# Kernel optimization log

Measured on AMD Instinct MI355X. Metric: run time of the kernel, lower is better.

Reference implementation:

```python
import jax, jax.numpy as jnp
import numpy as np

EPS = 1e-8


def setup_inputs() -> dict:
    key = jax.random.key(0)
    k1, k2, k3, k4 = jax.random.split(key, 4)
    b, c_in, c_out, h, w_, k = 16, 512, 512, 64, 64, 3
    return {
        "x": jax.random.normal(k1, (b, c_in, h, w_), dtype=jnp.float32),
        "w": jax.random.normal(k2, (b, 512), dtype=jnp.float32),
        "weight": jax.random.normal(k3, (c_out, c_in, k, k), dtype=jnp.float32),
        "affine_w": jax.random.normal(k4, (c_in, 512), dtype=jnp.float32) * 0.02,
        "affine_b": jnp.zeros((c_in,), dtype=jnp.float32),
    }


def reference(x, w, weight, affine_w, affine_b):
    # x: [b, c_in, h, w]; w: [b, 512]; weight: [c_out, c_in, k, k]
    b = x.shape[0]
    # per-sample modulation scale: [b, c_in]
    s = w @ affine_w.T + affine_b + 1.0
    # modulated weights: [b, c_out, c_in, k, k]
    wgt = weight[None] * s[:, None, :, None, None]
    # demodulation: rsqrt of sum over (c_in, kh, kw)
    d = jax.lax.rsqrt(jnp.sum(wgt ** 2, axis=(2, 3, 4)) + EPS)  # [b, c_out]
    wgt = wgt * d[:, :, None, None, None]

    def conv_one(x_i, w_i):
        # x_i: [c_in, h, w] -> [1, c_in, h, w]; w_i: [c_out, c_in, k, k]
        out = jax.lax.conv_general_dilated(
            x_i[None], w_i, window_strides=(1, 1), padding="SAME",
            dimension_numbers=("NCHW", "OIHW", "NCHW"))
        return out[0]

    return jax.vmap(conv_one)(x, wgt)  # [b, c_out, h, w]
```

## Files before the change

### kernel.cpp

```cpp
#include <hip/hip_runtime.h>
#include <cstdint>

typedef __bf16 bf16_t;
typedef __attribute__((ext_vector_type(8))) __bf16 bf16x8;
typedef __attribute__((ext_vector_type(4))) float f32x4;

#define MC_EPS 1e-8f

__device__ __forceinline__ void async_ld16(const bf16_t* g, bf16_t* l) {
  __builtin_amdgcn_global_load_lds(
      (const __attribute__((address_space(1))) void*)g,
      (__attribute__((address_space(3))) void*)l, 16, 0, 0);
}

__global__ void s_kernel(const float* __restrict__ w, const float* __restrict__ aw,
                         const float* __restrict__ ab, float* __restrict__ s) {
  int ci = blockIdx.x, tid = threadIdx.x;
  int b = tid >> 4, part = tid & 15;
  const float* ar = aw + (ci << 9);
  const float* wr = w + (b << 9);
  float acc = 0.f;
  for (int j = part; j < 512; j += 16) acc += wr[j] * ar[j];
  for (int off = 8; off; off >>= 1) acc += __shfl_down(acc, off, 64);
  if (part == 0) s[(b << 9) + ci] = acc + ab[ci] + 1.0f;
}

__global__ void prep_w_kernel(const float* __restrict__ wgt, float* __restrict__ wsq,
                              bf16_t* __restrict__ w_t) {
  int idx = blockIdx.x * 256 + threadIdx.x;
  const float* p = wgt + (size_t)idx * 9;
  float v[9];
  float a = 0.f;
#pragma unroll
  for (int j = 0; j < 9; ++j) { v[j] = p[j]; a += v[j] * v[j]; }
  wsq[idx] = a;
#pragma unroll
  for (int j = 0; j < 9; ++j) w_t[((size_t)j << 18) + idx] = (bf16_t)v[j];
}

__global__ void d_kernel(const float* __restrict__ wsq, const float* __restrict__ s,
                         float* __restrict__ d) {
  int co = blockIdx.x, tid = threadIdx.x;
  int b = tid >> 4, part = tid & 15;
  const float* wr = wsq + (co << 9);
  const float* sr = s + (b << 9);
  float acc = 0.f;
  for (int j = part; j < 512; j += 16) { float sv = sr[j]; acc += wr[j] * sv * sv; }
  for (int off = 8; off; off >>= 1) acc += __shfl_down(acc, off, 64);
  if (part == 0) d[(b << 9) + co] = rsqrtf(acc + MC_EPS);
}

__global__ void halo_kernel(bf16_t* __restrict__ xp) {
  int gid = blockIdx.x * 256 + threadIdx.x;
  if (gid >= 16 * 260 * 64) return;
  int cg = gid & 63;
  int p = (gid >> 6) % 260;
  int b = (gid >> 6) / 260;
  int h, w;
  if (p < 66)       { h = 0;       w = p; }
  else if (p < 132) { h = 65;      w = p - 66; }
  else if (p < 196) { h = p - 131; w = 0; }
  else              { h = p - 195; w = 65; }
  uint4 z = {0u, 0u, 0u, 0u};
  *(uint4*)&xp[((size_t)(b * 66 + h) * 66 + w) * 512 + (cg << 3)] = z;
}

__global__ void xmod_kernel(const float* __restrict__ x, const float* __restrict__ s,
                            bf16_t* __restrict__ xp) {
  int b = blockIdx.x >> 6, h = blockIdx.x & 63;
  int tid = threadIdx.x;
  __shared__ __align__(16) bf16_t tile[64 * 130];
  for (int c0 = 0; c0 < 512; c0 += 128) {
    if (c0) __syncthreads();
    int w4 = (tid & 15) << 2;
    int cl = tid >> 4;
#pragma unroll
    for (int r = 0; r < 8; ++r) {
      int ci = cl + (r << 4);
      const float4 v = *(const float4*)&x[(size_t)(((b << 9) + c0 + ci) << 12) + (h << 6) + w4];
      float sv = s[(b << 9) + c0 + ci];
      tile[(w4 + 0) * 130 + ci] = (bf16_t)(v.x * sv);
      tile[(w4 + 1) * 130 + ci] = (bf16_t)(v.y * sv);
      tile[(w4 + 2) * 130 + ci] = (bf16_t)(v.z * sv);
      tile[(w4 + 3) * 130 + ci] = (bf16_t)(v.w * sv);
    }
    __syncthreads();
#pragma unroll
    for (int it = 0; it < 4; ++it) {
      int i = tid + it * 256;
      int w = i >> 4, cg = i & 15;
      const uint32_t* tp = (const uint32_t*)&tile[w * 130 + (cg << 3)];
      uint4 v = { tp[0], tp[1], tp[2], tp[3] };
      *(uint4*)&xp[((size_t)(b * 66 + h + 1) * 66 + (w + 1)) * 512 + c0 + (cg << 3)] = v;
    }
  }
}

#define RDFRAG(SB, F)                                                           \
  { const int sbb_ = (SB);                                                      \
    _Pragma("unroll") for (int nt = 0; nt < 4; ++nt)                            \
      F[8 + nt] = *(const bf16x8*)&smem[sbb_ + 8192 + ((brow + (nt << 4)) << 5) + phys]; \
    _Pragma("unroll") for (int mt = 0; mt < 4; ++mt)                            \
      F[mt] = *(const bf16x8*)&smem[sbb_ + ((arow + (mt << 4)) << 5) + phys];   \
    _Pragma("unroll") for (int mt = 0; mt < 4; ++mt)                            \
      F[4 + mt] = *(const bf16x8*)&smem[sbb_ + ((arow + 64 + (mt << 4)) << 5) + phys]; }

#define TILE_STEP(K, FR, FW)                                                    \
  { const int k_ = (K);                                                         \
    if (k_ + 1 < 144) { RDFRAG(((k_ + 1) & 3) << 14, FW) }                      \
    if (k_ + 3 < 144) {                                                         \
      const int kp_ = k_ + 3;                                                   \
      const int pb_ = (kp_ & 3) << 14;                                          \
      const int tp_ = kp_ >> 4;                                                 \
      const int kh_ = tp_ / 3, kw_ = tp_ - kh_ * 3;                             \
      const int ao_ = ((kh_ * 66 + kw_) << 9) + ((kp_ & 15) << 5);              \
      const int bo_ = (tp_ << 18) + ((kp_ & 15) << 5);                          \
      async_ld16(xp + a_base[0] + ao_, &smem[pb_ + a_dst[0]]);                  \
      async_ld16(xp + a_base[1] + ao_, &smem[pb_ + a_dst[1]]);                  \
      async_ld16(w_t + b_base[0] + bo_, &smem[pb_ + b_dst[0]]);                 \
      async_ld16(w_t + b_base[1] + bo_, &smem[pb_ + b_dst[1]]);                 \
    }                                                                           \
    _Pragma("unroll") for (int mt = 0; mt < 4; ++mt)                            \
      _Pragma("unroll") for (int nt = 0; nt < 4; ++nt)                          \
        acc[mt][nt] = __builtin_amdgcn_mfma_f32_16x16x32_bf16(FR[mt], FR[8 + nt], acc[mt][nt], 0, 0, 0); \
    _Pragma("unroll") for (int mt = 0; mt < 4; ++mt)                            \
      _Pragma("unroll") for (int nt = 0; nt < 4; ++nt)                          \
        acc[4 + mt][nt] = __builtin_amdgcn_mfma_f32_16x16x32_bf16(FR[4 + mt], FR[8 + nt], acc[4 + mt][nt], 0, 0, 0); \
    if (k_ < 141) asm volatile("s_waitcnt vmcnt(4)" ::: "memory");              \
    else          asm volatile("s_waitcnt vmcnt(0)" ::: "memory");              \
    if (k_ < 143) __builtin_amdgcn_s_barrier(); }

__global__ __launch_bounds__(512, 2) void conv_kernel(
    const bf16_t* __restrict__ xp, const bf16_t* __restrict__ w_t,
    const float* __restrict__ d, float* __restrict__ out) {
  extern __shared__ bf16_t smem[];
  const int tid = threadIdx.x, lane = tid & 63;
  const int g = blockIdx.x;
  const int xcd = g & 7;
  const int slot = g >> 3;
  const int mb = (xcd << 5) + (slot >> 1);
  const int nb = slot & 1;
  const int b = mb >> 4;
  const int h0 = (mb & 15) << 2;
  const int n0 = nb << 8;
  const int wv = tid >> 6;
  const int wm = wv >> 2, wn = wv & 3;
  const int quad = lane >> 4, lr = lane & 15;

  int a_base[2], a_dst[2], b_base[2], b_dst[2];
#pragma unroll
  for (int j = 0; j < 2; ++j) {
    int e = (j << 9) + tid;
    int p = e >> 2;
    int cig = (e & 3) ^ ((p >> 1) & 3);
    a_base[j] = ((b * 66 + h0 + (p >> 6)) * 66 + (p & 63)) * 512 + (cig << 3);
    a_dst[j] = (e & ~63) << 3;
    b_base[j] = ((n0 + p) << 9) + (cig << 3);
    b_dst[j] = 8192 + a_dst[j];
  }

  f32x4 acc[8][4];
#pragma unroll
  for (int i = 0; i < 8; ++i)
#pragma unroll
    for (int j = 0; j < 4; ++j) acc[i][j] = (f32x4){0.f, 0.f, 0.f, 0.f};

#pragma unroll
  for (int kt = 0; kt < 3; ++kt) {
    const int cio = kt << 5;
    const int sb = kt << 14;
    async_ld16(xp + a_base[0] + cio, &smem[sb + a_dst[0]]);
    async_ld16(xp + a_base[1] + cio, &smem[sb + a_dst[1]]);
    async_ld16(w_t + b_base[0] + cio, &smem[sb + b_dst[0]]);
    async_ld16(w_t + b_base[1] + cio, &smem[sb + b_dst[1]]);
  }
  asm volatile("s_waitcnt vmcnt(4)" ::: "memory");
  __builtin_amdgcn_s_barrier();

  const int arow = (wm << 7) + lr;
  const int brow = (wn << 6) + lr;
  const int phys = (quad ^ ((lr >> 1) & 3)) << 3;

  bf16x8 fA[12], fB[12];
  RDFRAG(0, fA)

  for (int kk = 0; kk < 72; ++kk) {
    TILE_STEP(2 * kk,     fA, fB)
    TILE_STEP(2 * kk + 1, fB, fA)
  }

#pragma unroll
  for (int nt = 0; nt < 4; ++nt) {
    const int n = n0 + (wn << 6) + (nt << 4) + lr;
    const float dv = d[(b << 9) + n];
#pragma unroll
    for (int mt = 0; mt < 8; ++mt) {
#pragma unroll
      for (int r = 0; r < 4; ++r) {
        int m = (wm << 7) + (mt << 4) + (quad << 2) + r;
        int h = h0 + (m >> 6), w = m & 63;
        out[((size_t)((b << 9) + n) << 12) + (h << 6) + w] = acc[mt][nt][r] * dv;
      }
    }
  }
}

extern "C" void kernel_launch(void* const* d_in, const int* in_sizes, int n_in,
                              void* d_out, int out_size, void* d_ws, size_t ws_size,
                              hipStream_t stream) {
  const float* x      = (const float*)d_in[0];
  const float* w      = (const float*)d_in[1];
  const float* weight = (const float*)d_in[2];
  const float* aw     = (const float*)d_in[3];
  const float* ab     = (const float*)d_in[4];
  float* out = (float*)d_out;

  char* ws = (char*)d_ws;
  const size_t XP_BYTES  = (size_t)16 * 66 * 66 * 512 * 2;
  const size_t WT_BYTES  = (size_t)9 * 512 * 512 * 2;
  bf16_t* xp   = (bf16_t*)ws;
  bf16_t* w_t  = (bf16_t*)(ws + XP_BYTES);
  float*  s    = (float*)(ws + XP_BYTES + WT_BYTES);
  float*  wsq  = (float*)(ws + XP_BYTES + WT_BYTES + 32768);
  float*  dbuf = (float*)(ws + XP_BYTES + WT_BYTES + 32768 + 1048576);

  static int attr_done = 0;
  if (!attr_done) {
    hipFuncSetAttribute(reinterpret_cast<const void*>(conv_kernel),
                        hipFuncAttributeMaxDynamicSharedMemorySize, 131072);
    attr_done = 1;
  }

  halo_kernel<<<1040, 256, 0, stream>>>(xp);
  s_kernel<<<512, 256, 0, stream>>>(w, aw, ab, s);
  prep_w_kernel<<<1024, 256, 0, stream>>>(weight, wsq, w_t);
  d_kernel<<<512, 256, 0, stream>>>(wsq, s, dbuf);
  xmod_kernel<<<1024, 256, 0, stream>>>(x, s, xp);
  conv_kernel<<<512, 512, 131072, stream>>>(xp, w_t, dbuf, out);
}
```

Measured before the change: 507.3 us.

## Use 4 waves per block with 128x128 warp tiles in conv GEMM

Halves the threads per conv block from 512 to 256 and gives each wave a 128x128 output tile (8x8 MFMA accumulators) instead of 128x64. Each thread now issues 8 async loads per k-step instead of 4, and the vmcnt waits are adjusted to match. The goal is more MFMA work per LDS fragment read, giving better register-level reuse and fewer LDS reads per FLOP. The cost is heavy register pressure (256 accumulator VGPRs plus double-buffered fragments) and fewer waves to hide latency, since launch_bounds drops to one 256-thread block.

```diff
diff --git a/kernel.cpp b/kernel.cpp
--- a/kernel.cpp
+++ b/kernel.cpp
@@ -96,18 +96,16 @@
   }
 }
 
-#define RDFRAG(SB, F)                                                           \
+#define RDFRAG(SB, FA, FB)                                                      \
   { const int sbb_ = (SB);                                                      \
-    _Pragma("unroll") for (int nt = 0; nt < 4; ++nt)                            \
-      F[8 + nt] = *(const bf16x8*)&smem[sbb_ + 8192 + ((brow + (nt << 4)) << 5) + phys]; \
-    _Pragma("unroll") for (int mt = 0; mt < 4; ++mt)                            \
-      F[mt] = *(const bf16x8*)&smem[sbb_ + ((arow + (mt << 4)) << 5) + phys];   \
-    _Pragma("unroll") for (int mt = 0; mt < 4; ++mt)                            \
-      F[4 + mt] = *(const bf16x8*)&smem[sbb_ + ((arow + 64 + (mt << 4)) << 5) + phys]; }
-
-#define TILE_STEP(K, FR, FW)                                                    \
+    _Pragma("unroll") for (int nt = 0; nt < 8; ++nt)                            \
+      FB[nt] = *(const bf16x8*)&smem[sbb_ + 8192 + ((brow + (nt << 4)) << 5) + phys]; \
+    _Pragma("unroll") for (int mt = 0; mt < 8; ++mt)                            \
+      FA[mt] = *(const bf16x8*)&smem[sbb_ + ((arow + (mt << 4)) << 5) + phys]; }
+
+#define TILE_STEP(K, AR, BR, AW, BW)                                            \
   { const int k_ = (K);                                                         \
-    if (k_ + 1 < 144) { RDFRAG(((k_ + 1) & 3) << 14, FW) }                      \
+    if (k_ + 1 < 144) { RDFRAG(((k_ + 1) & 3) << 14, AW, BW) }                  \
     if (k_ + 3 < 144) {                                                         \
       const int kp_ = k_ + 3;                                                   \
       const int pb_ = (kp_ & 3) << 14;                                          \
@@ -115,22 +113,19 @@
       const int kh_ = tp_ / 3, kw_ = tp_ - kh_ * 3;                             \
       const int ao_ = ((kh_ * 66 + kw_) << 9) + ((kp_ & 15) << 5);              \
       const int bo_ = (tp_ << 18) + ((kp_ & 15) << 5);                          \
-      async_ld16(xp + a_base[0] + ao_, &smem[pb_ + a_dst[0]]);                  \
-      async_ld16(xp + a_base[1] + ao_, &smem[pb_ + a_dst[1]]);                  \
-      async_ld16(w_t + b_base[0] + bo_, &smem[pb_ + b_dst[0]]);                 \
-      async_ld16(w_t + b_base[1] + bo_, &smem[pb_ + b_dst[1]]);                 \
+      _Pragma("unroll") for (int j = 0; j < 4; ++j) {                           \
+        async_ld16(xp + a_base[j] + ao_, &smem[pb_ + a_dst[j]]);                \
+        async_ld16(w_t + b_base[j] + bo_, &smem[pb_ + b_dst[j]]);               \
+      }                                                                         \
     }                                                                           \
-    _Pragma("unroll") for (int mt = 0; mt < 4; ++mt)                            \
-      _Pragma("unroll") for (int nt = 0; nt < 4; ++nt)                          \
-        acc[mt][nt] = __builtin_amdgcn_mfma_f32_16x16x32_bf16(FR[mt], FR[8 + nt], acc[mt][nt], 0, 0, 0); \
-    _Pragma("unroll") for (int mt = 0; mt < 4; ++mt)                            \
-      _Pragma("unroll") for (int nt = 0; nt < 4; ++nt)                          \
-        acc[4 + mt][nt] = __builtin_amdgcn_mfma_f32_16x16x32_bf16(FR[4 + mt], FR[8 + nt], acc[4 + mt][nt], 0, 0, 0); \
-    if (k_ < 141) asm volatile("s_waitcnt vmcnt(4)" ::: "memory");              \
+    _Pragma("unroll") for (int mt = 0; mt < 8; ++mt)                            \
+      _Pragma("unroll") for (int nt = 0; nt < 8; ++nt)                          \
+        acc[mt][nt] = __builtin_amdgcn_mfma_f32_16x16x32_bf16(AR[mt], BR[nt], acc[mt][nt], 0, 0, 0); \
+    if (k_ < 141) asm volatile("s_waitcnt vmcnt(8)" ::: "memory");              \
     else          asm volatile("s_waitcnt vmcnt(0)" ::: "memory");              \
     if (k_ < 143) __builtin_amdgcn_s_barrier(); }
 
-__global__ __launch_bounds__(512, 2) void conv_kernel(
+__global__ __launch_bounds__(256, 1) void conv_kernel(
     const bf16_t* __restrict__ xp, const bf16_t* __restrict__ w_t,
     const float* __restrict__ d, float* __restrict__ out) {
   extern __shared__ bf16_t smem[];
@@ -144,13 +139,13 @@
   const int h0 = (mb & 15) << 2;
   const int n0 = nb << 8;
   const int wv = tid >> 6;
-  const int wm = wv >> 2, wn = wv & 3;
+  const int wm = wv >> 1, wn = wv & 1;
   const int quad = lane >> 4, lr = lane & 15;
 
-  int a_base[2], a_dst[2], b_base[2], b_dst[2];
-#pragma unroll
-  for (int j = 0; j < 2; ++j) {
-    int e = (j << 9) + tid;
+  int a_base[4], a_dst[4], b_base[4], b_dst[4];
+#pragma unroll
+  for (int j = 0; j < 4; ++j) {
+    int e = (j << 8) + tid;
     int p = e >> 2;
     int cig = (e & 3) ^ ((p >> 1) & 3);
     a_base[j] = ((b * 66 + h0 + (p >> 6)) * 66 + (p & 63)) * 512 + (cig << 3);
@@ -159,39 +154,40 @@
     b_dst[j] = 8192 + a_dst[j];
   }
 
-  f32x4 acc[8][4];
+  f32x4 acc[8][8];
 #pragma unroll
   for (int i = 0; i < 8; ++i)
 #pragma unroll
-    for (int j = 0; j < 4; ++j) acc[i][j] = (f32x4){0.f, 0.f, 0.f, 0.f};
+    for (int j = 0; j < 8; ++j) acc[i][j] = (f32x4){0.f, 0.f, 0.f, 0.f};
 
 #pragma unroll
   for (int kt = 0; kt < 3; ++kt) {
     const int cio = kt << 5;
     const int sb = kt << 14;
-    async_ld16(xp + a_base[0] + cio, &smem[sb + a_dst[0]]);
-    async_ld16(xp + a_base[1] + cio, &smem[sb + a_dst[1]]);
-    async_ld16(w_t + b_base[0] + cio, &smem[sb + b_dst[0]]);
-    async_ld16(w_t + b_base[1] + cio, &smem[sb + b_dst[1]]);
-  }
-  asm volatile("s_waitcnt vmcnt(4)" ::: "memory");
+#pragma unroll
+    for (int j = 0; j < 4; ++j) {
+      async_ld16(xp + a_base[j] + cio, &smem[sb + a_dst[j]]);
+      async_ld16(w_t + b_base[j] + cio, &smem[sb + b_dst[j]]);
+    }
+  }
+  asm volatile("s_waitcnt vmcnt(8)" ::: "memory");
   __builtin_amdgcn_s_barrier();
 
   const int arow = (wm << 7) + lr;
-  const int brow = (wn << 6) + lr;
+  const int brow = (wn << 7) + lr;
   const int phys = (quad ^ ((lr >> 1) & 3)) << 3;
 
-  bf16x8 fA[12], fB[12];
-  RDFRAG(0, fA)
+  bf16x8 fa0[8], fb0[8], fa1[8], fb1[8];
+  RDFRAG(0, fa0, fb0)
 
   for (int kk = 0; kk < 72; ++kk) {
-    TILE_STEP(2 * kk,     fA, fB)
-    TILE_STEP(2 * kk + 1, fB, fA)
-  }
-
-#pragma unroll
-  for (int nt = 0; nt < 4; ++nt) {
-    const int n = n0 + (wn << 6) + (nt << 4) + lr;
+    TILE_STEP(2 * kk,     fa0, fb0, fa1, fb1)
+    TILE_STEP(2 * kk + 1, fa1, fb1, fa0, fb0)
+  }
+
+#pragma unroll
+  for (int nt = 0; nt < 8; ++nt) {
+    const int n = n0 + (wn << 7) + (nt << 4) + lr;
     const float dv = d[(b << 9) + n];
 #pragma unroll
     for (int mt = 0; mt < 8; ++mt) {
@@ -236,5 +232,5 @@
   prep_w_kernel<<<1024, 256, 0, stream>>>(weight, wsq, w_t);
   d_kernel<<<512, 256, 0, stream>>>(wsq, s, dbuf);
   xmod_kernel<<<1024, 256, 0, stream>>>(x, s, xp);
-  conv_kernel<<<512, 512, 131072, stream>>>(xp, w_t, dbuf, out);
-}
+  conv_kernel<<<512, 256, 131072, stream>>>(xp, w_t, dbuf, out);
+}
```

Measured after the change: 589.6 us. 1.16x slower.

## Restructure conv main loop into K=64 double-buffered, four-phase ping-pong schedule

Applied to the files above, without the earlier changes.

Replaces the 4-stage K=32 pipeline with a 2-buffer K=64 tile pipeline (72 iterations). Each iteration is split into four quadrant phases that interleave LDS fragment reads, async global-to-LDS loads and MFMA blocks, separated by barriers and s_setprio. The LDS swizzle and layout change to 64-element rows with an XOR over 8 chunks, and launch bounds drop to 1 block per CU. The aim is to overlap memory with MFMA work and cut barrier overhead per FLOP, at the risk of lower occupancy and more barriers per iteration.

```diff
diff --git a/kernel.cpp b/kernel.cpp
--- a/kernel.cpp
+++ b/kernel.cpp
@@ -96,41 +96,42 @@
   }
 }
 
-#define RDFRAG(SB, F)                                                           \
-  { const int sbb_ = (SB);                                                      \
-    _Pragma("unroll") for (int nt = 0; nt < 4; ++nt)                            \
-      F[8 + nt] = *(const bf16x8*)&smem[sbb_ + 8192 + ((brow + (nt << 4)) << 5) + phys]; \
-    _Pragma("unroll") for (int mt = 0; mt < 4; ++mt)                            \
-      F[mt] = *(const bf16x8*)&smem[sbb_ + ((arow + (mt << 4)) << 5) + phys];   \
-    _Pragma("unroll") for (int mt = 0; mt < 4; ++mt)                            \
-      F[4 + mt] = *(const bf16x8*)&smem[sbb_ + ((arow + 64 + (mt << 4)) << 5) + phys]; }
-
-#define TILE_STEP(K, FR, FW)                                                    \
-  { const int k_ = (K);                                                         \
-    if (k_ + 1 < 144) { RDFRAG(((k_ + 1) & 3) << 14, FW) }                      \
-    if (k_ + 3 < 144) {                                                         \
-      const int kp_ = k_ + 3;                                                   \
-      const int pb_ = (kp_ & 3) << 14;                                          \
-      const int tp_ = kp_ >> 4;                                                 \
-      const int kh_ = tp_ / 3, kw_ = tp_ - kh_ * 3;                             \
-      const int ao_ = ((kh_ * 66 + kw_) << 9) + ((kp_ & 15) << 5);              \
-      const int bo_ = (tp_ << 18) + ((kp_ & 15) << 5);                          \
-      async_ld16(xp + a_base[0] + ao_, &smem[pb_ + a_dst[0]]);                  \
-      async_ld16(xp + a_base[1] + ao_, &smem[pb_ + a_dst[1]]);                  \
-      async_ld16(w_t + b_base[0] + bo_, &smem[pb_ + b_dst[0]]);                 \
-      async_ld16(w_t + b_base[1] + bo_, &smem[pb_ + b_dst[1]]);                 \
-    }                                                                           \
-    _Pragma("unroll") for (int mt = 0; mt < 4; ++mt)                            \
-      _Pragma("unroll") for (int nt = 0; nt < 4; ++nt)                          \
-        acc[mt][nt] = __builtin_amdgcn_mfma_f32_16x16x32_bf16(FR[mt], FR[8 + nt], acc[mt][nt], 0, 0, 0); \
-    _Pragma("unroll") for (int mt = 0; mt < 4; ++mt)                            \
-      _Pragma("unroll") for (int nt = 0; nt < 4; ++nt)                          \
-        acc[4 + mt][nt] = __builtin_amdgcn_mfma_f32_16x16x32_bf16(FR[4 + mt], FR[8 + nt], acc[4 + mt][nt], 0, 0, 0); \
-    if (k_ < 141) asm volatile("s_waitcnt vmcnt(4)" ::: "memory");              \
-    else          asm volatile("s_waitcnt vmcnt(0)" ::: "memory");              \
-    if (k_ < 143) __builtin_amdgcn_s_barrier(); }
-
-__global__ __launch_bounds__(512, 2) void conv_kernel(
+#define RD_A(QM)                                                                \
+  _Pragma("unroll") for (int mt = 0; mt < 4; ++mt)                              \
+    _Pragma("unroll") for (int ks = 0; ks < 2; ++ks)                            \
+      fa[mt * 2 + ks] = *(const bf16x8*)&smem[cb +                              \
+        (((wm << 7) + ((QM) << 6) + (mt << 4) + lr) << 6) +                     \
+        ((((ks << 2) | quad) ^ lr7) << 3)];
+
+#define RD_B(QN, FB)                                                            \
+  _Pragma("unroll") for (int nt = 0; nt < 2; ++nt)                              \
+    _Pragma("unroll") for (int ks = 0; ks < 2; ++ks)                            \
+      FB[nt * 2 + ks] = *(const bf16x8*)&smem[cb + 16384 +                      \
+        (((wn << 6) + ((QN) << 5) + (nt << 4) + lr) << 6) +                     \
+        ((((ks << 2) | quad) ^ lr7) << 3)];
+
+#define ST_A(C)                                                                 \
+  if (pf) { async_ld16(xp + aab[C][0] + aoff, &smem[ob + aad[C][0]]);           \
+            async_ld16(xp + aab[C][1] + aoff, &smem[ob + aad[C][1]]); }
+
+#define ST_B(C)                                                                 \
+  if (pf) { async_ld16(w_t + bbb[C][0] + boff, &smem[ob + bbd[C][0]]);          \
+            async_ld16(w_t + bbb[C][1] + boff, &smem[ob + bbd[C][1]]); }
+
+#define MM(FB, RB, CB)                                                          \
+  _Pragma("unroll") for (int mt = 0; mt < 4; ++mt)                              \
+    _Pragma("unroll") for (int nt = 0; nt < 2; ++nt)                            \
+      _Pragma("unroll") for (int ks = 0; ks < 2; ++ks)                          \
+        acc[(RB) + mt][(CB) + nt] = __builtin_amdgcn_mfma_f32_16x16x32_bf16(    \
+            fa[mt * 2 + ks], FB[nt * 2 + ks], acc[(RB) + mt][(CB) + nt], 0, 0, 0);
+
+#define BAR1()                                                                  \
+  __builtin_amdgcn_s_barrier();                                                 \
+  asm volatile("s_waitcnt lgkmcnt(0)" ::: "memory");                            \
+  __builtin_amdgcn_sched_barrier(0);                                            \
+  __builtin_amdgcn_s_setprio(1);
+
+__global__ __launch_bounds__(512, 1) void conv_kernel(
     const bf16_t* __restrict__ xp, const bf16_t* __restrict__ w_t,
     const float* __restrict__ d, float* __restrict__ out) {
   extern __shared__ bf16_t smem[];
@@ -145,19 +146,24 @@
   const int n0 = nb << 8;
   const int wv = tid >> 6;
   const int wm = wv >> 2, wn = wv & 3;
-  const int quad = lane >> 4, lr = lane & 15;
-
-  int a_base[2], a_dst[2], b_base[2], b_dst[2];
-#pragma unroll
-  for (int j = 0; j < 2; ++j) {
-    int e = (j << 9) + tid;
-    int p = e >> 2;
-    int cig = (e & 3) ^ ((p >> 1) & 3);
-    a_base[j] = ((b * 66 + h0 + (p >> 6)) * 66 + (p & 63)) * 512 + (cig << 3);
-    a_dst[j] = (e & ~63) << 3;
-    b_base[j] = ((n0 + p) << 9) + (cig << 3);
-    b_dst[j] = 8192 + a_dst[j];
-  }
+  const int quad = lane >> 4, lr = lane & 15, lr7 = lr & 7;
+
+  int aab[2][2], aad[2][2], bbb[2][2], bbd[2][2];
+#pragma unroll
+  for (int c = 0; c < 2; ++c)
+#pragma unroll
+    for (int j = 0; j < 2; ++j) {
+      int e = (j << 9) + tid;
+      int r = e >> 3;
+      int cig = e & 7;
+      int kk = cig ^ (r & 7);
+      int px = ((r >> 6) << 7) + (c << 6) + (r & 63);
+      aab[c][j] = ((b * 66 + h0 + (px >> 6)) * 66 + (px & 63)) * 512 + (kk << 3);
+      aad[c][j] = (px << 6) + (cig << 3);
+      int co = ((r >> 5) << 6) + (c << 5) + (r & 31);
+      bbb[c][j] = ((n0 + co) << 9) + (kk << 3);
+      bbd[c][j] = 16384 + (co << 6) + (cig << 3);
+    }
 
   f32x4 acc[8][4];
 #pragma unroll
@@ -165,28 +171,58 @@
 #pragma unroll
     for (int j = 0; j < 4; ++j) acc[i][j] = (f32x4){0.f, 0.f, 0.f, 0.f};
 
-#pragma unroll
-  for (int kt = 0; kt < 3; ++kt) {
-    const int cio = kt << 5;
-    const int sb = kt << 14;
-    async_ld16(xp + a_base[0] + cio, &smem[sb + a_dst[0]]);
-    async_ld16(xp + a_base[1] + cio, &smem[sb + a_dst[1]]);
-    async_ld16(w_t + b_base[0] + cio, &smem[sb + b_dst[0]]);
-    async_ld16(w_t + b_base[1] + cio, &smem[sb + b_dst[1]]);
+  {
+    const bool pf = true; const int ob = 0, aoff = 0, boff = 0;
+    ST_A(0) ST_B(0) ST_B(1) ST_A(1)
   }
   asm volatile("s_waitcnt vmcnt(4)" ::: "memory");
   __builtin_amdgcn_s_barrier();
 
-  const int arow = (wm << 7) + lr;
-  const int brow = (wn << 6) + lr;
-  const int phys = (quad ^ ((lr >> 1) & 3)) << 3;
-
-  bf16x8 fA[12], fB[12];
-  RDFRAG(0, fA)
-
-  for (int kk = 0; kk < 72; ++kk) {
-    TILE_STEP(2 * kk,     fA, fB)
-    TILE_STEP(2 * kk + 1, fB, fA)
+  bf16x8 fa[8], fb0[4], fb1[4];
+
+  for (int t = 0; t < 72; ++t) {
+    const int cb = (t & 1) << 15;
+    const int ob = cb ^ 32768;
+    const int tn = t + 1;
+    const bool pf = tn < 72;
+    const int tap = tn >> 3;
+    const int kh = tap / 3, kw = tap - kh * 3;
+    const int ci0 = (tn & 7) << 6;
+    const int aoff = ((kh * 66 + kw) << 9) + ci0;
+    const int boff = (tap << 18) + ci0;
+
+    RD_A(0) RD_B(0, fb0)
+    ST_A(0)
+    BAR1()
+    MM(fb0, 0, 0)
+    __builtin_amdgcn_s_setprio(0);
+    if (t < 71) asm volatile("s_waitcnt vmcnt(4)" ::: "memory");
+    else        asm volatile("s_waitcnt vmcnt(2)" ::: "memory");
+    __builtin_amdgcn_s_barrier();
+
+    RD_B(1, fb1)
+    ST_B(0)
+    BAR1()
+    MM(fb1, 0, 2)
+    __builtin_amdgcn_s_setprio(0);
+    if (t < 71) asm volatile("s_waitcnt vmcnt(4)" ::: "memory");
+    else        asm volatile("s_waitcnt vmcnt(0)" ::: "memory");
+    __builtin_amdgcn_s_barrier();
+
+    RD_A(1)
+    ST_B(1)
+    BAR1()
+    MM(fb1, 4, 2)
+    __builtin_amdgcn_s_setprio(0);
+    __builtin_amdgcn_s_barrier();
+
+    ST_A(1)
+    __builtin_amdgcn_s_barrier();
+    __builtin_amdgcn_s_setprio(1);
+    MM(fb0, 4, 0)
+    __builtin_amdgcn_s_setprio(0);
+    if (t < 71) asm volatile("s_waitcnt vmcnt(4)" ::: "memory");
+    __builtin_amdgcn_s_barrier();
   }
 
 #pragma unroll
```

Result: no change. 505.5 us (-0.4%).
